# Kernel tuning notes

Measured on AMD Instinct MI355X. Metric: run time of the kernel, lower is better.

## Reference

```python
import jax, jax.numpy as jnp
import numpy as np
from jax.ops import segment_sum, segment_min, segment_max

N, E = 25000, 400000
NF, EF = 30, 10
H = 40          # n_hidden (multiple of towers)
T = 5           # towers
F = H           # F_in per tower (divide_input=False)
FO = H // T     # F_out per tower
L = 2           # gnn layers
NC = 2          # classes
EPS_BN = 1e-5


def setup_inputs() -> dict:
    key = jax.random.key(0)
    ks = jax.random.split(key, 24)
    r = lambda k, s, sc=0.1: jax.random.normal(k, s, jnp.float32) * sc
    return {
        "x": jax.random.normal(ks[0], (N, NF), jnp.float32),
        "edge_attr": jax.random.normal(ks[1], (E, EF), jnp.float32),
        "edge_index": jax.random.randint(ks[2], (2, E), 0, N, jnp.int32),
        "node_w": r(ks[3], (NF, H)), "node_b": r(ks[4], (H,)),
        "edge_w": r(ks[5], (EF, H)), "edge_b": r(ks[6], (H,)),
        "enc_w": r(ks[7], (L, H, F)), "enc_b": r(ks[8], (L, F)),
        "pre_w": r(ks[9], (L, T, 3 * F, F)), "pre_b": r(ks[10], (L, T, F)),
        "post_w": r(ks[11], (L, T, 13 * F, FO)), "post_b": r(ks[12], (L, T, FO)),
        "lin_w": r(ks[13], (L, H, H)), "lin_b": r(ks[14], (L, H)),
        "bn_g": jnp.ones((L, H), jnp.float32), "bn_b": jnp.zeros((L, H), jnp.float32),
        "mlp1_w": r(ks[15], (3 * H, 50)), "mlp1_b": r(ks[16], (50,)),
        "mlp2_w": r(ks[17], (50, 25)), "mlp2_b": r(ks[18], (25,)),
        "mlp3_w": r(ks[19], (25, NC)), "mlp3_b": r(ks[20], (NC,)),
    }


def _pna_conv(x, src, dst, e_emb, enc_w, enc_b, pre_w, pre_b, post_w, post_b,
              lin_w, lin_b, cnt, cnt1, amp, att):
    # message: per-tower pre-MLP on cat(x_i=dst, x_j=src, enc(edge_attr))
    e = e_emb @ enc_w + enc_b                                    # [E, F]
    h = jnp.concatenate([x[dst], x[src], e], axis=-1)            # [E, 3F]
    hs = jnp.einsum('ef,tfo->eto', h, pre_w) + pre_b             # [E, T, F]
    # multi-aggregation over incoming edges (index = dst)
    c = cnt1[:, None, None]
    mean = segment_sum(hs, dst, num_segments=N) / c
    msq = segment_sum(hs * hs, dst, num_segments=N) / c
    std = jnp.sqrt(jax.nn.relu(msq - mean * mean) + 1e-5)
    has = (cnt > 0)[:, None, None]
    mn = jnp.where(has, segment_min(hs, dst, num_segments=N), 0.0)
    mx = jnp.where(has, segment_max(hs, dst, num_segments=N), 0.0)
    agg = jnp.concatenate([mean, mn, mx, std], axis=-1)          # [N, T, 4F]
    agg = jnp.concatenate([agg, agg * amp, agg * att], axis=-1)  # [N, T, 12F]
    out = jnp.concatenate(
        [jnp.broadcast_to(x[:, None, :], (N, T, F)), agg], axis=-1)  # [N, T, 13F]
    out = jnp.einsum('ntf,tfo->nto', out, post_w) + post_b       # [N, T, FO]
    return out.reshape(N, T * FO) @ lin_w + lin_b                # [N, H]


def reference(x, edge_attr, node_w, node_b, edge_w, edge_b, enc_w, enc_b,
              pre_w, pre_b, post_w, post_b, lin_w, lin_b, bn_g, bn_b,
              mlp1_w, mlp1_b, mlp2_w, mlp2_b, mlp3_w, mlp3_b, edge_index):
    src, dst = edge_index[0], edge_index[1]
    cnt = segment_sum(jnp.ones((E,), jnp.float32), dst, num_segments=N)  # in-degree
    cnt1 = jnp.maximum(cnt, 1.0)                                 # deg.clamp_(1)
    log_deg = jnp.log(cnt1 + 1.0)
    avg_log = jnp.mean(jnp.log(cnt + 1.0))                       # PNA avg_deg['log']
    amp = (log_deg / avg_log)[:, None, None]
    att = (avg_log / log_deg)[:, None, None]
    h = x @ node_w + node_b                                      # node embedding
    e_emb = edge_attr @ edge_w + edge_b                          # edge embedding
    for i in range(L):
        c = _pna_conv(h, src, dst, e_emb, enc_w[i], enc_b[i], pre_w[i], pre_b[i],
                      post_w[i], post_b[i], lin_w[i], lin_b[i], cnt, cnt1, amp, att)
        mu = jnp.mean(c, axis=0)
        var = jnp.mean((c - mu) ** 2, axis=0)                    # BatchNorm (batch stats)
        cbn = (c - mu) / jnp.sqrt(var + EPS_BN) * bn_g[i] + bn_b[i]
        h = (h + jax.nn.relu(cbn)) / 2.0
    z = jax.nn.relu(jnp.concatenate([h[src], h[dst]], axis=-1))  # [E, 2H]
    z = jnp.concatenate([z, e_emb], axis=-1)                     # [E, 3H]
    z = jax.nn.relu(z @ mlp1_w + mlp1_b)
    z = jax.nn.relu(z @ mlp2_w + mlp2_b)
    return z @ mlp3_w + mlp3_b                                   # [E, NC]
```

## Files before the change

### kernel.cpp

```cpp
#include <hip/hip_runtime.h>
#include <hip/hip_bf16.h>
#include <cstdint>
#include <cstddef>

#define NN 25000
#define NE 400000
#define NFD 30
#define EFD 10
#define H 40
#define T 5
#define FO 8
#define LAYERS 2
#define TF 200
#define PSTR 52
#define REC 12
#define WCN 416
#define WCK 64
#define SHP 72
#define EPSV 1e-5f

typedef __attribute__((ext_vector_type(8))) short bf16x8;
typedef __attribute__((ext_vector_type(4))) float f32x4;

__device__ inline short bfbits(float v) {
    __hip_bfloat16 b = __float2bfloat16(v);
    return *(short*)&b;
}

__global__ __launch_bounds__(256) void k_deg(const int* __restrict__ dst, int* __restrict__ cnt) {
    int e = blockIdx.x * 256 + threadIdx.x;
    if (e < NE) atomicAdd(&cnt[dst[e]], 1);
}

__global__ __launch_bounds__(256) void k_avglog(const int* __restrict__ cnt, float* __restrict__ slot) {
    __shared__ float red[256];
    float s = 0.0f;
    for (int i = blockIdx.x * 256 + threadIdx.x; i < NN; i += gridDim.x * 256)
        s += logf((float)cnt[i] + 1.0f);
    red[threadIdx.x] = s; __syncthreads();
    for (int o = 128; o > 0; o >>= 1) {
        if (threadIdx.x < o) red[threadIdx.x] += red[threadIdx.x + o];
        __syncthreads();
    }
    if (threadIdx.x == 0) atomicAdd(slot, red[0]);
}

__global__ __launch_bounds__(256) void k_node(const float* __restrict__ x, const float* __restrict__ w,
                                              const float* __restrict__ b, float* __restrict__ h,
                                              const int* __restrict__ cnt, const float* __restrict__ slot,
                                              float* __restrict__ amp, float* __restrict__ att) {
    int id = blockIdx.x * 256 + threadIdx.x;
    if (id < NN) {
        float avg = slot[0] / (float)NN;
        float c1 = fmaxf((float)cnt[id], 1.0f);
        float lg = logf(c1 + 1.0f);
        amp[id] = lg / avg;
        att[id] = avg / lg;
    }
    if (id >= NN * H) return;
    int n = id / H, j = id - n * H;
    const float* xr = x + (size_t)n * NFD;
    float acc = b[j];
    #pragma unroll
    for (int m = 0; m < NFD; m++) acc += xr[m] * w[m * H + j];
    h[id] = acc;
}

__global__ __launch_bounds__(1024) void k_scan(const int* __restrict__ cnt, int* __restrict__ offs) {
    __shared__ int wsum[16];
    int tid = threadIdx.x;
    int lane = tid & 63, wv = tid >> 6;
    int runbase = 0;
    for (int base = 0; base < NN; base += 4096) {
        int i0 = base + tid * 4;
        int4 v = make_int4(0, 0, 0, 0);
        if (i0 < NN) v = *(const int4*)(cnt + i0);
        int tsum = v.x + v.y + v.z + v.w;
        int x = tsum;
        #pragma unroll
        for (int o = 1; o < 64; o <<= 1) {
            int y = __shfl_up(x, o);
            if (lane >= o) x += y;
        }
        if (lane == 63) wsum[wv] = x;
        __syncthreads();
        if (wv == 0 && lane < 16) {
            int wsv = wsum[lane];
            #pragma unroll
            for (int o = 1; o < 16; o <<= 1) {
                int y = __shfl_up(wsv, o);
                if (lane >= o) wsv += y;
            }
            wsum[lane] = wsv;
        }
        __syncthreads();
        int wpref = (wv > 0) ? wsum[wv - 1] : 0;
        int excl = runbase + wpref + x - tsum;
        if (i0 < NN) {
            offs[i0]     = excl;
            offs[i0 + 1] = excl + v.x;
            offs[i0 + 2] = excl + v.x + v.y;
            offs[i0 + 3] = excl + v.x + v.y + v.z;
        }
        runbase += wsum[15];
        __syncthreads();
    }
    if (tid == 0) offs[NN] = runbase;
}

__global__ __launch_bounds__(256) void k_scatter(const int* __restrict__ src, const int* __restrict__ dst,
                                                 const float* __restrict__ edge_attr,
                                                 const int* __restrict__ offs, int* __restrict__ fill,
                                                 float* __restrict__ ea_csr, int* __restrict__ pdst) {
    int e = blockIdx.x * 256 + threadIdx.x;
    if (e >= NE) return;
    int d = dst[e];
    int p = offs[d] + atomicAdd(&fill[d], 1);
    const float2* ear = (const float2*)(edge_attr + (size_t)e * EFD);
    float2 v0 = ear[0], v1 = ear[1], v2 = ear[2], v3 = ear[3], v4 = ear[4];
    float4* o = (float4*)(ea_csr + (size_t)p * REC);
    o[0] = make_float4(v0.x, v0.y, v1.x, v1.y);
    o[1] = make_float4(v2.x, v2.y, v3.x, v3.y);
    o[2] = make_float4(v4.x, v4.y, __int_as_float(src[e]), __int_as_float(e));
    pdst[p] = d;
}

__global__ __launch_bounds__(256) void k_prep1(const float* __restrict__ enc_w, const float* __restrict__ enc_b,
                                               const float* __restrict__ edge_w, const float* __restrict__ edge_b,
                                               const float* __restrict__ pre_w, const float* __restrict__ pre_b,
                                               const float* __restrict__ post_w,
                                               const float* __restrict__ w1, const float* __restrict__ b1,
                                               float* __restrict__ W3e, float* __restrict__ dvecF,
                                               __hip_bfloat16* __restrict__ Wcat,
                                               float* __restrict__ Wp4, float* __restrict__ Wxd,
                                               float* __restrict__ W1e, float* __restrict__ b1e, int layer) {
    int id = blockIdx.x * 256 + threadIdx.x;
    const int B0 = EFD * TF;
    const int B1 = B0 + WCN * WCK;
    const int B2 = B1 + EFD * 50;
    const int B3 = B2 + 40 * 512;
    const int B4 = B3 + H * H;
    if (id < B0) {
        int m = id / TF, j = id - m * TF;
        int t = j / H, f = j - t * H;
        const float* ew = enc_w + (size_t)layer * H * H;
        const float* pw = pre_w + (size_t)(layer * T + t) * 120 * H;
        float acc = 0.0f;
        for (int k = 0; k < H; k++) {
            float wk = edge_w[m * H + k];
            float g = 0.0f;
            #pragma unroll
            for (int o = 0; o < H; o++) g += ew[k * H + o] * pw[(80 + o) * H + f];
            acc += wk * g;
        }
        W3e[m * TF + j] = acc;
        if (m == 0) {
            const float* eb = enc_b + (size_t)layer * H;
            float dacc = pre_b[(size_t)(layer * T + t) * H + f];
            for (int o = 0; o < H; o++) {
                float ebe = eb[o];
                #pragma unroll
                for (int k = 0; k < H; k++) ebe += edge_b[k] * ew[k * H + o];
                dacc += ebe * pw[(80 + o) * H + f];
            }
            dvecF[j] = dacc;
        }
    } else if (id < B1) {
        int id2 = id - B0;
        int j = id2 / WCK, k = id2 - j * WCK;
        float val = 0.0f;
        if (k < H) {
            if (j < TF) {
                int t = j / H, f = j - t * H;
                val = pre_w[((size_t)(layer * T + t) * 120 + k) * H + f];
            } else if (j >= 208 && j < 208 + TF) {
                int j2 = j - 208;
                int t = j2 / H, f = j2 - t * H;
                val = pre_w[((size_t)(layer * T + t) * 120 + H + k) * H + f];
            }
        }
        Wcat[id2] = __float2bfloat16(val);
    } else if (id < B2) {
        if (layer == 0) {
            int id2 = id - B1;
            int m = id2 / 50, o = id2 - m * 50;
            float acc = 0.0f;
            #pragma unroll
            for (int k = 0; k < H; k++) acc += edge_w[m * H + k] * w1[(80 + k) * 50 + o];
            W1e[m * 50 + o] = acc;
            if (m == 0) {
                float bacc = b1[o];
                #pragma unroll
                for (int k = 0; k < H; k++) bacc += edge_b[k] * w1[(80 + k) * 50 + o];
                b1e[o] = bacc;
            }
        }
    } else if (id < B3) {
        int i2 = id - B2;
        int fs4 = i2 >> 9;
        int rem = i2 & 511;
        int col = rem >> 2, c = rem & 3;
        int fs = fs4 * 4 + c;
        float v = 0.0f;
        if (col < 120) {
            int t = col / 24, r2 = col - t * 24;
            int grp = r2 >> 3, o = r2 & 7;
            v = post_w[((size_t)(layer * T + t) * 520 + 40 + grp * 160 + fs) * FO + o];
        }
        Wp4[i2] = v;
    } else if (id < B4) {
        int i2 = id - B3;
        int j = i2 / H, f = i2 - j * H;
        int t = j >> 3, o = j & 7;
        Wxd[i2] = post_w[((size_t)(layer * T + t) * 520 + f) * FO + o];
    }
}

__global__ __launch_bounds__(256) void k_abm(float* h, const float* __restrict__ cbuf,
                                             const float* __restrict__ bnsum, const float* __restrict__ bnsq,
                                             const float* __restrict__ bng, const float* __restrict__ bnb,
                                             int doBN,
                                             const __hip_bfloat16* __restrict__ Wcat,
                                             float* __restrict__ A, __hip_bfloat16* __restrict__ Bbf) {
    __shared__ short sh[64 * SHP];
    int tid = threadIdx.x;
    int n0 = blockIdx.x * 64;
    int nodes = NN - n0; if (nodes > 64) nodes = 64;
    for (int i = tid; i < 64 * SHP; i += 256) sh[i] = 0;
    __syncthreads();
    float invN = 1.0f / (float)NN;
    for (int i = tid; i < nodes * H; i += 256) {
        int f = i % H;
        float hv = h[(size_t)n0 * H + i];
        float hn;
        if (doBN) {
            float mu = bnsum[f] * invN;
            float var = bnsq[f] * invN - mu * mu;
            float c = (cbuf[(size_t)n0 * H + i] - mu) * rsqrtf(var + EPSV) * bng[f] + bnb[f];
            hn = (hv + fmaxf(c, 0.0f)) * 0.5f;
            h[(size_t)n0 * H + i] = hn;
        } else {
            hn = hv;
        }
        sh[(i / H) * SHP + f] = bfbits(hn);
    }
    __syncthreads();

    int wv = tid >> 6, lane = tid & 63;
    int q = lane >> 4, c16 = lane & 15;
    const short* arow = sh + (wv * 16 + c16) * SHP + q * 8;
    bf16x8 a0 = *(const bf16x8*)(arow);
    bf16x8 a1 = *(const bf16x8*)(arow + 32);
    int gm = n0 + wv * 16 + q * 4;

    for (int jt = 0; jt < 26; jt++) {
        int col = jt * 16 + c16;
        const short* wrow = (const short*)Wcat + (size_t)col * WCK + q * 8;
        bf16x8 b0 = *(const bf16x8*)(wrow);
        bf16x8 b1 = *(const bf16x8*)(wrow + 32);
        f32x4 acc = {0.0f, 0.0f, 0.0f, 0.0f};
        acc = __builtin_amdgcn_mfma_f32_16x16x32_bf16(a0, b0, acc, 0, 0, 0);
        acc = __builtin_amdgcn_mfma_f32_16x16x32_bf16(a1, b1, acc, 0, 0, 0);
        if (col < TF) {
            #pragma unroll
            for (int r = 0; r < 4; r++) {
                int row = gm + r;
                if (row < NN) A[(size_t)row * TF + col] = acc[r];
            }
        } else if (col >= 208) {
            int c2 = col - 208;
            if (c2 < TF) {
                #pragma unroll
                for (int r = 0; r < 4; r++) {
                    int row = gm + r;
                    if (row < NN) Bbf[(size_t)row * TF + c2] = __float2bfloat16(acc[r]);
                }
            }
        }
    }
}

__global__ __launch_bounds__(256) void k_agg(const float* __restrict__ ea_csr,
                                             const __hip_bfloat16* __restrict__ Bbf,
                                             const float* __restrict__ A, const float* __restrict__ w3e,
                                             const float* __restrict__ dvecF, const int* __restrict__ cnt,
                                             const int* __restrict__ offs,
                                             const float* __restrict__ h,
                                             const float* __restrict__ Wp4, const float* __restrict__ Wxd,
                                             const float* __restrict__ pbL,
                                             const float* __restrict__ amp, const float* __restrict__ att,
                                             float* __restrict__ cpre) {
    __shared__ float sst[4 * 800];
    __shared__ float spart[4 * 120];
    __shared__ float shh[4 * H];
    int tid = threadIdx.x;
    int lane = tid & 63;
    int wv = tid >> 6;
    int n0 = blockIdx.x * 4;
    int n = __builtin_amdgcn_readfirstlane(n0 + wv);
    if (tid < 4 * H) shh[tid] = h[(size_t)n0 * H + tid];
    int deg = cnt[n];
    int start = offs[n];
    bool comp = lane < TF / 4;
    float4 w3q[EFD];
    float4 dj4 = make_float4(0, 0, 0, 0), a4 = make_float4(0, 0, 0, 0);
    if (comp) {
        #pragma unroll
        for (int m = 0; m < EFD; m++) w3q[m] = *(const float4*)(w3e + m * TF + 4 * lane);
        dj4 = *(const float4*)(dvecF + 4 * lane);
        a4  = *(const float4*)(A + (size_t)n * TF + 4 * lane);
    }
    float sx = 0, sy = 0, sz = 0, sw_ = 0;
    float qx = 0, qy = 0, qz = 0, qw = 0;
    float mnx = 3.4e38f, mny = 3.4e38f, mnz = 3.4e38f, mnw = 3.4e38f;
    float mxx = -3.4e38f, mxy = -3.4e38f, mxz = -3.4e38f, mxw = -3.4e38f;
    const float4* recb = (const float4*)ea_csr + (size_t)start * 3;
    const uint16_t* Bu = (const uint16_t*)Bbf;

    auto edge = [&](float4 qa, float4 qb, float4 qc, uint2 bv) {
        float b0 = __uint_as_float(bv.x << 16);
        float b1 = __uint_as_float(bv.x & 0xffff0000u);
        float b2 = __uint_as_float(bv.y << 16);
        float b3 = __uint_as_float(bv.y & 0xffff0000u);
        float eav[EFD] = {qa.x, qa.y, qa.z, qa.w, qb.x, qb.y, qb.z, qb.w, qc.x, qc.y};
        float cx = dj4.x, cy = dj4.y, cz = dj4.z, cw = dj4.w;
        #pragma unroll
        for (int m = 0; m < EFD; m++) {
            cx = fmaf(eav[m], w3q[m].x, cx);
            cy = fmaf(eav[m], w3q[m].y, cy);
            cz = fmaf(eav[m], w3q[m].z, cz);
            cw = fmaf(eav[m], w3q[m].w, cw);
        }
        float ux = b0 + cx, uy = b1 + cy, uz = b2 + cz, uw = b3 + cw;
        sx += ux; qx = fmaf(ux, ux, qx); mnx = fminf(mnx, ux); mxx = fmaxf(mxx, ux);
        sy += uy; qy = fmaf(uy, uy, qy); mny = fminf(mny, uy); mxy = fmaxf(mxy, uy);
        sz += uz; qz = fmaf(uz, uz, qz); mnz = fminf(mnz, uz); mxz = fmaxf(mxz, uz);
        sw_ += uw; qw = fmaf(uw, uw, qw); mnw = fminf(mnw, uw); mxw = fmaxf(mxw, uw);
    };

    int r = 0;
    for (; r + 4 <= deg; r += 4) {
        float4 qa0 = recb[(r + 0) * 3], qb0 = recb[(r + 0) * 3 + 1], qc0 = recb[(r + 0) * 3 + 2];
        float4 qa1 = recb[(r + 1) * 3], qb1 = recb[(r + 1) * 3 + 1], qc1 = recb[(r + 1) * 3 + 2];
        float4 qa2 = recb[(r + 2) * 3], qb2 = recb[(r + 2) * 3 + 1], qc2 = recb[(r + 2) * 3 + 2];
        float4 qa3 = recb[(r + 3) * 3], qb3 = recb[(r + 3) * 3 + 1], qc3 = recb[(r + 3) * 3 + 2];
        int s0 = __float_as_int(qc0.z), s1 = __float_as_int(qc1.z);
        int s2 = __float_as_int(qc2.z), s3 = __float_as_int(qc3.z);
        if (comp) {
            uint2 v0 = *(const uint2*)(Bu + (size_t)s0 * TF + 4 * lane);
            uint2 v1 = *(const uint2*)(Bu + (size_t)s1 * TF + 4 * lane);
            uint2 v2 = *(const uint2*)(Bu + (size_t)s2 * TF + 4 * lane);
            uint2 v3 = *(const uint2*)(Bu + (size_t)s3 * TF + 4 * lane);
            edge(qa0, qb0, qc0, v0);
            edge(qa1, qb1, qc1, v1);
            edge(qa2, qb2, qc2, v2);
            edge(qa3, qb3, qc3, v3);
        }
    }
    for (; r < deg; r++) {
        float4 qa = recb[r * 3], qb = recb[r * 3 + 1], qc = recb[r * 3 + 2];
        int sn = __float_as_int(qc.z);
        if (comp) {
            uint2 bv = *(const uint2*)(Bu + (size_t)sn * TF + 4 * lane);
            edge(qa, qb, qc, bv);
        }
    }
    if (comp) {
        float d = (float)deg, c1 = fmaxf(d, 1.0f);
        float inv = 1.0f / c1;
        float mex = (d * a4.x + sx) * inv, mey = (d * a4.y + sy) * inv;
        float mez = (d * a4.z + sz) * inv, mew = (d * a4.w + sw_) * inv;
        float msx = (d * a4.x * a4.x + 2.0f * a4.x * sx + qx) * inv;
        float msy = (d * a4.y * a4.y + 2.0f * a4.y * sy + qy) * inv;
        float msz = (d * a4.z * a4.z + 2.0f * a4.z * sz + qz) * inv;
        float msw = (d * a4.w * a4.w + 2.0f * a4.w * sw_ + qw) * inv;
        float4 mean4 = make_float4(mex, mey, mez, mew);
        float4 sd4 = make_float4(sqrtf(fmaxf(msx - mex * mex, 0.0f) + EPSV),
                                 sqrtf(fmaxf(msy - mey * mey, 0.0f) + EPSV),
                                 sqrtf(fmaxf(msz - mez * mez, 0.0f) + EPSV),
                                 sqrtf(fmaxf(msw - mew * mew, 0.0f) + EPSV));
        bool has = deg > 0;
        float4 mnv4 = has ? make_float4(a4.x + mnx, a4.y + mny, a4.z + mnz, a4.w + mnw)
                          : make_float4(0, 0, 0, 0);
        float4 mxv4 = has ? make_float4(a4.x + mxx, a4.y + mxy, a4.z + mxz, a4.w + mxw)
                          : make_float4(0, 0, 0, 0);
        int j0 = 4 * lane;
        int t = j0 / H, f = j0 - t * H;
        float* sb = sst + wv * 800 + t * 160 + f;
        *(float4*)(sb)       = mean4;
        *(float4*)(sb + 40)  = mnv4;
        *(float4*)(sb + 80)  = mxv4;
        *(float4*)(sb + 120) = sd4;
    }
    __syncthreads();

    {
        int op = tid & 127, g = tid >> 7;
        int tt = op / 24; if (tt > 4) tt = 4;
        const float* sa = sst + (g * 2) * 800 + tt * 160;
        const float* sb = sa + 800;
        float pa = 0.0f, pb = 0.0f;
        #pragma unroll 4
        for (int fs4 = 0; fs4 < 40; fs4++) {
            float4 w  = *(const float4*)(Wp4 + fs4 * 512 + op * 4);
            float4 va = *(const float4*)(sa + fs4 * 4);
            float4 vb = *(const float4*)(sb + fs4 * 4);
            pa += va.x * w.x + va.y * w.y + va.z * w.z + va.w * w.w;
            pb += vb.x * w.x + vb.y * w.y + vb.z * w.z + vb.w * w.w;
        }
        if (op < 120) {
            spart[(g * 2) * 120 + op]     = pa;
            spart[(g * 2 + 1) * 120 + op] = pb;
        }
    }
    __syncthreads();

    if (tid < 160) {
        int nd = tid / H, j = tid - nd * H;
        int t = j >> 3, o = j & 7;
        int ng = n0 + nd;
        float am = amp[ng], at = att[ng];
        const float* yr = spart + nd * 120 + t * 24 + o;
        float acc = pbL[j] + yr[0] + am * yr[8] + at * yr[16];
        const float* hr = shh + nd * H;
        const float* wx = Wxd + (size_t)j * H;
        #pragma unroll
        for (int fq = 0; fq < 10; fq++) {
            float4 hv = *(const float4*)(hr + fq * 4);
            float4 wv = *(const float4*)(wx + fq * 4);
            acc += hv.x * wv.x + hv.y * wv.y + hv.z * wv.z + hv.w * wv.w;
        }
        cpre[(size_t)ng * H + j] = acc;
    }
}

__global__ __launch_bounds__(256) void k_linbn(const float* __restrict__ cpre, const float* __restrict__ lin_w,
                                               const float* __restrict__ lin_b, float* __restrict__ cbuf,
                                               float* __restrict__ bnsum, float* __restrict__ bnsq, int layer) {
    __shared__ float scp[240];
    __shared__ float red[80];
    int tid = threadIdx.x;
    int j = tid % H, nl = tid / H;
    const float* lw = lin_w + (size_t)layer * H * H;
    float wcol[H];
    #pragma unroll
    for (int k = 0; k < H; k++) wcol[k] = lw[k * H + j];
    float lb = lin_b[(size_t)layer * H + j];
    float lsum = 0.0f, lsq = 0.0f;
    for (int n0 = blockIdx.x * 6; n0 < NN; n0 += gridDim.x * 6) {
        int nn = NN - n0; if (nn > 6) nn = 6;
        if (tid < nn * H) scp[tid] = cpre[(size_t)n0 * H + tid];
        __syncthreads();
        if (nl < nn) {
            float acc = lb;
            #pragma unroll
            for (int k = 0; k < H; k++) acc += scp[nl * H + k] * wcol[k];
            cbuf[(size_t)(n0 + nl) * H + j] = acc;
            lsum += acc; lsq += acc * acc;
        }
        __syncthreads();
    }
    if (tid < 80) red[tid] = 0.0f;
    __syncthreads();
    if (nl < 6) { atomicAdd(&red[j], lsum); atomicAdd(&red[40 + j], lsq); }
    __syncthreads();
    if (tid < 40) atomicAdd(&bnsum[tid], red[tid]);
    else if (tid < 80) atomicAdd(&bnsq[tid - 40], red[tid]);
}

__global__ __launch_bounds__(256) void k_prep2(const float* __restrict__ h, const float* __restrict__ cbuf,
                                               const float* __restrict__ bnsum, const float* __restrict__ bnsq,
                                               const float* __restrict__ bng, const float* __restrict__ bnb,
                                               const float* __restrict__ w1,
                                               float* __restrict__ P1, float* __restrict__ P2) {
    __shared__ float sh[5 * H];
    int tid = threadIdx.x;
    int n0 = blockIdx.x * 5;
    if (tid < 5 * H) {
        int j = tid % H;
        float invN = 1.0f / (float)NN;
        float mu = bnsum[j] * invN;
        float var = bnsq[j] * invN - mu * mu;
        float inv = rsqrtf(var + EPSV);
        float cv = (cbuf[(size_t)n0 * H + tid] - mu) * inv * bng[j] + bnb[j];
        sh[tid] = (h[(size_t)n0 * H + tid] + fmaxf(cv, 0.0f)) * 0.5f;
    }
    __syncthreads();
    if (tid >= 250) return;
    int nl = tid / 50, o = tid - nl * 50;
    const float* hr = sh + nl * H;
    float a1 = 0.0f, a2 = 0.0f;
    #pragma unroll
    for (int f = 0; f < H; f++) {
        float v = fmaxf(hr[f], 0.0f);
        a1 += v * w1[f * 50 + o];
        a2 += v * w1[(H + f) * 50 + o];
    }
    P1[(size_t)(n0 + nl) * PSTR + o] = a1;
    P2[(size_t)(n0 + nl) * PSTR + o] = a2;
}

__global__ __launch_bounds__(256) void k_mlp(const float* __restrict__ ea_csr, const int* __restrict__ pdst,
                                             const float* __restrict__ P1, const float* __restrict__ P2,
                                             const float* __restrict__ W1e, const float* __restrict__ b1e,
                                             const float* __restrict__ w2, const float* __restrict__ b2,
                                             const float* __restrict__ w3, const float* __restrict__ b3,
                                             float* __restrict__ out) {
    int p = blockIdx.x * 256 + threadIdx.x;
    if (p >= NE) return;
    const float4* rec = (const float4*)ea_csr + (size_t)p * 3;
    float4 r0 = rec[0], r1 = rec[1], r2 = rec[2];
    int s = __float_as_int(r2.z), eid = __float_as_int(r2.w);
    int d = pdst[p];
    float ea[EFD] = {r0.x, r0.y, r0.z, r0.w, r1.x, r1.y, r1.z, r1.w, r2.x, r2.y};

    float z1[52];
    const float4* p1r = (const float4*)(P1 + (size_t)s * PSTR);
    const float4* p2r = (const float4*)(P2 + (size_t)d * PSTR);
    #pragma unroll
    for (int i = 0; i < 13; i++) {
        float4 a = p1r[i], b = p2r[i];
        z1[4 * i]     = a.x + b.x;
        z1[4 * i + 1] = a.y + b.y;
        z1[4 * i + 2] = a.z + b.z;
        z1[4 * i + 3] = a.w + b.w;
    }
    #pragma unroll
    for (int k = 0; k < 50; k++) z1[k] += b1e[k];
    #pragma unroll
    for (int m = 0; m < EFD; m++) {
        float v = ea[m];
        #pragma unroll
        for (int k = 0; k < 50; k++) z1[k] = fmaf(v, W1e[m * 50 + k], z1[k]);
    }
    float z2[25];
    #pragma unroll
    for (int o = 0; o < 25; o++) z2[o] = b2[o];
    #pragma unroll
    for (int k = 0; k < 50; k++) {
        float v = fmaxf(z1[k], 0.0f);
        #pragma unroll
        for (int o = 0; o < 25; o++) z2[o] = fmaf(v, w2[k * 25 + o], z2[o]);
    }
    float o0 = b3[0], o1 = b3[1];
    #pragma unroll
    for (int k = 0; k < 25; k++) {
        float v = fmaxf(z2[k], 0.0f);
        o0 = fmaf(v, w3[k * 2], o0);
        o1 = fmaf(v, w3[k * 2 + 1], o1);
    }
    *(float2*)(out + (size_t)eid * 2) = make_float2(o0, o1);
}

extern "C" void kernel_launch(void* const* d_in, const int* in_sizes, int n_in,
                              void* d_out, int out_size, void* d_ws, size_t ws_size,
                              hipStream_t stream) {
    const float* x         = (const float*)d_in[0];
    const float* edge_attr = (const float*)d_in[1];
    const int*   eidx      = (const int*)  d_in[2];
    const float* node_w    = (const float*)d_in[3];
    const float* node_b    = (const float*)d_in[4];
    const float* edge_w    = (const float*)d_in[5];
    const float* edge_b    = (const float*)d_in[6];
    const float* enc_w     = (const float*)d_in[7];
    const float* enc_b     = (const float*)d_in[8];
    const float* pre_w     = (const float*)d_in[9];
    const float* pre_b     = (const float*)d_in[10];
    const float* post_w    = (const float*)d_in[11];
    const float* post_b    = (const float*)d_in[12];
    const float* lin_w     = (const float*)d_in[13];
    const float* lin_b     = (const float*)d_in[14];
    const float* bn_g      = (const float*)d_in[15];
    const float* bn_b      = (const float*)d_in[16];
    const float* w1 = (const float*)d_in[17];
    const float* b1 = (const float*)d_in[18];
    const float* w2 = (const float*)d_in[19];
    const float* b2 = (const float*)d_in[20];
    const float* w3 = (const float*)d_in[21];
    const float* b3 = (const float*)d_in[22];
    const int* srcp = eidx;
    const int* dstp = eidx + NE;
    float* out = (float*)d_out;

    char* ws = (char*)d_ws;
    size_t off = 0;
    auto alloc = [&](size_t bytes) -> char* {
        char* p = ws + off;
        off += (bytes + 255) & ~(size_t)255;
        return p;
    };
    float* h      = (float*)alloc((size_t)NN * H * 4);
    float* Abuf   = (float*)alloc((size_t)NN * TF * 4);
    float* cbuf   = (float*)alloc((size_t)NN * H * 4);
    __hip_bfloat16* Bbf = (__hip_bfloat16*)alloc((size_t)NN * TF * 2 + 256);
    float* cpre   = (float*)alloc((size_t)NN * H * 4);
    float* ea_csr = (float*)alloc((size_t)NE * REC * 4);
    int* pdst     = (int*)alloc((size_t)NE * 4);
    float* W3e    = (float*)alloc((size_t)EFD * TF * 4);
    float* dvecF  = (float*)alloc((size_t)TF * 4);
    __hip_bfloat16* Wcat = (__hip_bfloat16*)alloc((size_t)WCN * WCK * 2);
    float* Wp4    = (float*)alloc((size_t)40 * 512 * 4);
    float* Wxd    = (float*)alloc((size_t)H * H * 4);
    float* P1     = (float*)alloc((size_t)NN * PSTR * 4);
    float* P2     = (float*)alloc((size_t)NN * PSTR * 4);
    float* W1e    = (float*)alloc((size_t)EFD * 50 * 4);
    float* b1e    = (float*)alloc((size_t)64 * 4);
    float* amp    = (float*)alloc((size_t)NN * 4);
    float* att    = (float*)alloc((size_t)NN * 4);
    int* offs     = (int*)alloc((size_t)(NN + 1) * 4);
    size_t zoff = off;
    int* cnt_i    = (int*)alloc((size_t)NN * 4);
    int* fill     = (int*)alloc((size_t)NN * 4);
    float* avgs   = (float*)alloc(256);
    float* bnz    = (float*)alloc(1024);
    size_t zsize = off - zoff;
    if (off > ws_size) return;

    hipMemsetAsync(cnt_i, 0, zsize, stream);

    k_deg<<<(NE + 255) / 256, 256, 0, stream>>>(dstp, cnt_i);
    k_avglog<<<64, 256, 0, stream>>>(cnt_i, avgs);
    k_node<<<(NN * H + 255) / 256, 256, 0, stream>>>(x, node_w, node_b, h, cnt_i, avgs, amp, att);
    k_scan<<<1, 1024, 0, stream>>>(cnt_i, offs);
    k_scatter<<<(NE + 255) / 256, 256, 0, stream>>>(srcp, dstp, edge_attr, offs, fill, ea_csr, pdst);

    int prep1_tot = EFD * TF + WCN * WCK + EFD * 50 + 40 * 512 + H * H;
    int prep1_grid = (prep1_tot + 255) / 256;
    for (int layer = 0; layer < LAYERS; layer++) {
        float* bnzL = bnz + layer * 128;
        k_prep1<<<prep1_grid, 256, 0, stream>>>(
            enc_w, enc_b, edge_w, edge_b, pre_w, pre_b, post_w, w1, b1,
            W3e, dvecF, Wcat, Wp4, Wxd, W1e, b1e, layer);
        float* bnzP = bnz + (layer - 1) * 128;
        k_abm<<<(NN + 63) / 64, 256, 0, stream>>>(
            h, cbuf, (layer > 0) ? bnzP : bnz, (layer > 0) ? bnzP + 40 : bnz,
            bn_g + (size_t)(layer > 0 ? layer - 1 : 0) * H,
            bn_b + (size_t)(layer > 0 ? layer - 1 : 0) * H,
            (layer > 0) ? 1 : 0, Wcat, Abuf, Bbf);
        k_agg<<<NN / 4, 256, 0, stream>>>(ea_csr, Bbf, Abuf, W3e, dvecF, cnt_i, offs,
                                          h, Wp4, Wxd, post_b + (size_t)layer * T * FO,
                                          amp, att, cpre);
        k_linbn<<<1024, 256, 0, stream>>>(cpre, lin_w, lin_b, cbuf, bnzL, bnzL + 40, layer);
    }
    k_prep2<<<NN / 5, 256, 0, stream>>>(h, cbuf, bnz + 128, bnz + 168,
                                        bn_g + H, bn_b + H, w1, P1, P2);
    k_mlp<<<(NE + 255) / 256, 256, 0, stream>>>(ea_csr, pdst, P1, P2, W1e, b1e, w2, b2, w3, b3, out);
}
```

Baseline: 583.8 us.

## Process eight nodes per aggregation block to amortize post-MLP weight loads

The aggregation kernel now has each wavefront handle two destination nodes in sequence, so a block covers eight nodes instead of four. The post-tower weight matrix Wp4 is then read once per eight nodes, with the K dimension split across two thread halves and partial sums reduced through shared memory reused from the stats buffer. The cost is serialized per-wave edge loops, which means less latency hiding from parallel nodes. Shared memory also grows, and fewer blocks are launched, which could lower occupancy.

Result: no change. 586.1 us (+0.4%).

```diff
diff --git a/kernel.cpp b/kernel.cpp
--- a/kernel.cpp
+++ b/kernel.cpp
@@ -17,6 +17,7 @@
 #define WCN 416
 #define WCK 64
 #define SHP 72
+#define NPB 8
 #define EPSV 1e-5f
 
 typedef __attribute__((ext_vector_type(8))) short bf16x8;
@@ -290,138 +291,165 @@
                                              const float* __restrict__ pbL,
                                              const float* __restrict__ amp, const float* __restrict__ att,
                                              float* __restrict__ cpre) {
-    __shared__ float sst[4 * 800];
-    __shared__ float spart[4 * 120];
-    __shared__ float shh[4 * H];
+    __shared__ float sst[NPB * 800];
+    __shared__ float shh[NPB * H];
+    float* spart = sst;
     int tid = threadIdx.x;
     int lane = tid & 63;
     int wv = tid >> 6;
-    int n0 = blockIdx.x * 4;
-    int n = __builtin_amdgcn_readfirstlane(n0 + wv);
-    if (tid < 4 * H) shh[tid] = h[(size_t)n0 * H + tid];
-    int deg = cnt[n];
-    int start = offs[n];
+    int n0 = blockIdx.x * NPB;
+    for (int idx = tid; idx < NPB * H; idx += 256) shh[idx] = h[(size_t)n0 * H + idx];
     bool comp = lane < TF / 4;
     float4 w3q[EFD];
-    float4 dj4 = make_float4(0, 0, 0, 0), a4 = make_float4(0, 0, 0, 0);
+    float4 dj4 = make_float4(0, 0, 0, 0);
     if (comp) {
         #pragma unroll
         for (int m = 0; m < EFD; m++) w3q[m] = *(const float4*)(w3e + m * TF + 4 * lane);
         dj4 = *(const float4*)(dvecF + 4 * lane);
-        a4  = *(const float4*)(A + (size_t)n * TF + 4 * lane);
-    }
-    float sx = 0, sy = 0, sz = 0, sw_ = 0;
-    float qx = 0, qy = 0, qz = 0, qw = 0;
-    float mnx = 3.4e38f, mny = 3.4e38f, mnz = 3.4e38f, mnw = 3.4e38f;
-    float mxx = -3.4e38f, mxy = -3.4e38f, mxz = -3.4e38f, mxw = -3.4e38f;
-    const float4* recb = (const float4*)ea_csr + (size_t)start * 3;
+    }
     const uint16_t* Bu = (const uint16_t*)Bbf;
 
-    auto edge = [&](float4 qa, float4 qb, float4 qc, uint2 bv) {
-        float b0 = __uint_as_float(bv.x << 16);
-        float b1 = __uint_as_float(bv.x & 0xffff0000u);
-        float b2 = __uint_as_float(bv.y << 16);
-        float b3 = __uint_as_float(bv.y & 0xffff0000u);
-        float eav[EFD] = {qa.x, qa.y, qa.z, qa.w, qb.x, qb.y, qb.z, qb.w, qc.x, qc.y};
-        float cx = dj4.x, cy = dj4.y, cz = dj4.z, cw = dj4.w;
-        #pragma unroll
-        for (int m = 0; m < EFD; m++) {
-            cx = fmaf(eav[m], w3q[m].x, cx);
-            cy = fmaf(eav[m], w3q[m].y, cy);
-            cz = fmaf(eav[m], w3q[m].z, cz);
-            cw = fmaf(eav[m], w3q[m].w, cw);
-        }
-        float ux = b0 + cx, uy = b1 + cy, uz = b2 + cz, uw = b3 + cw;
-        sx += ux; qx = fmaf(ux, ux, qx); mnx = fminf(mnx, ux); mxx = fmaxf(mxx, ux);
-        sy += uy; qy = fmaf(uy, uy, qy); mny = fminf(mny, uy); mxy = fmaxf(mxy, uy);
-        sz += uz; qz = fmaf(uz, uz, qz); mnz = fminf(mnz, uz); mxz = fmaxf(mxz, uz);
-        sw_ += uw; qw = fmaf(uw, uw, qw); mnw = fminf(mnw, uw); mxw = fmaxf(mxw, uw);
-    };
-
-    int r = 0;
-    for (; r + 4 <= deg; r += 4) {
-        float4 qa0 = recb[(r + 0) * 3], qb0 = recb[(r + 0) * 3 + 1], qc0 = recb[(r + 0) * 3 + 2];
-        float4 qa1 = recb[(r + 1) * 3], qb1 = recb[(r + 1) * 3 + 1], qc1 = recb[(r + 1) * 3 + 2];
-        float4 qa2 = recb[(r + 2) * 3], qb2 = recb[(r + 2) * 3 + 1], qc2 = recb[(r + 2) * 3 + 2];
-        float4 qa3 = recb[(r + 3) * 3], qb3 = recb[(r + 3) * 3 + 1], qc3 = recb[(r + 3) * 3 + 2];
-        int s0 = __float_as_int(qc0.z), s1 = __float_as_int(qc1.z);
-        int s2 = __float_as_int(qc2.z), s3 = __float_as_int(qc3.z);
+    for (int i = 0; i < 2; i++) {
+        int n = __builtin_amdgcn_readfirstlane(n0 + wv * 2 + i);
+        int deg = cnt[n];
+        int start = offs[n];
+        float4 a4 = make_float4(0, 0, 0, 0);
+        if (comp) a4 = *(const float4*)(A + (size_t)n * TF + 4 * lane);
+        float sx = 0, sy = 0, sz = 0, sw_ = 0;
+        float qx = 0, qy = 0, qz = 0, qw = 0;
+        float mnx = 3.4e38f, mny = 3.4e38f, mnz = 3.4e38f, mnw = 3.4e38f;
+        float mxx = -3.4e38f, mxy = -3.4e38f, mxz = -3.4e38f, mxw = -3.4e38f;
+        const float4* recb = (const float4*)ea_csr + (size_t)start * 3;
+
+        auto edge = [&](float4 qa, float4 qb, float4 qc, uint2 bv) {
+            float b0 = __uint_as_float(bv.x << 16);
+            float b1 = __uint_as_float(bv.x & 0xffff0000u);
+            float b2 = __uint_as_float(bv.y << 16);
+            float b3 = __uint_as_float(bv.y & 0xffff0000u);
+            float eav[EFD] = {qa.x, qa.y, qa.z, qa.w, qb.x, qb.y, qb.z, qb.w, qc.x, qc.y};
+            float cx = dj4.x, cy = dj4.y, cz = dj4.z, cw = dj4.w;
+            #pragma unroll
+            for (int m = 0; m < EFD; m++) {
+                cx = fmaf(eav[m], w3q[m].x, cx);
+                cy = fmaf(eav[m], w3q[m].y, cy);
+                cz = fmaf(eav[m], w3q[m].z, cz);
+                cw = fmaf(eav[m], w3q[m].w, cw);
+            }
+            float ux = b0 + cx, uy = b1 + cy, uz = b2 + cz, uw = b3 + cw;
+            sx += ux; qx = fmaf(ux, ux, qx); mnx = fminf(mnx, ux); mxx = fmaxf(mxx, ux);
+            sy += uy; qy = fmaf(uy, uy, qy); mny = fminf(mny, uy); mxy = fmaxf(mxy, uy);
+            sz += uz; qz = fmaf(uz, uz, qz); mnz = fminf(mnz, uz); mxz = fmaxf(mxz, uz);
+            sw_ += uw; qw = fmaf(uw, uw, qw); mnw = fminf(mnw, uw); mxw = fmaxf(mxw, uw);
+        };
+
+        int r = 0;
+        for (; r + 4 <= deg; r += 4) {
+            float4 qa0 = recb[(r + 0) * 3], qb0 = recb[(r + 0) * 3 + 1], qc0 = recb[(r + 0) * 3 + 2];
+            float4 qa1 = recb[(r + 1) * 3], qb1 = recb[(r + 1) * 3 + 1], qc1 = recb[(r + 1) * 3 + 2];
+            float4 qa2 = recb[(r + 2) * 3], qb2 = recb[(r + 2) * 3 + 1], qc2 = recb[(r + 2) * 3 + 2];
+            float4 qa3 = recb[(r + 3) * 3], qb3 = recb[(r + 3) * 3 + 1], qc3 = recb[(r + 3) * 3 + 2];
+            int s0 = __float_as_int(qc0.z), s1 = __float_as_int(qc1.z);
+            int s2 = __float_as_int(qc2.z), s3 = __float_as_int(qc3.z);
+            if (comp) {
+                uint2 v0 = *(const uint2*)(Bu + (size_t)s0 * TF + 4 * lane);
+                uint2 v1 = *(const uint2*)(Bu + (size_t)s1 * TF + 4 * lane);
+                uint2 v2 = *(const uint2*)(Bu + (size_t)s2 * TF + 4 * lane);
+                uint2 v3 = *(const uint2*)(Bu + (size_t)s3 * TF + 4 * lane);
+                edge(qa0, qb0, qc0, v0);
+                edge(qa1, qb1, qc1, v1);
+                edge(qa2, qb2, qc2, v2);
+                edge(qa3, qb3, qc3, v3);
+            }
+        }
+        for (; r < deg; r++) {
+            float4 qa = recb[r * 3], qb = recb[r * 3 + 1], qc = recb[r * 3 + 2];
+            int sn = __float_as_int(qc.z);
+            if (comp) {
+                uint2 bv = *(const uint2*)(Bu + (size_t)sn * TF + 4 * lane);
+                edge(qa, qb, qc, bv);
+            }
+        }
         if (comp) {
-            uint2 v0 = *(const uint2*)(Bu + (size_t)s0 * TF + 4 * lane);
-            uint2 v1 = *(const uint2*)(Bu + (size_t)s1 * TF + 4 * lane);
-            uint2 v2 = *(const uint2*)(Bu + (size_t)s2 * TF + 4 * lane);
-            uint2 v3 = *(const uint2*)(Bu + (size_t)s3 * TF + 4 * lane);
-            edge(qa0, qb0, qc0, v0);
-            edge(qa1, qb1, qc1, v1);
-            edge(qa2, qb2, qc2, v2);
-            edge(qa3, qb3, qc3, v3);
-        }
-    }
-    for (; r < deg; r++) {
-        float4 qa = recb[r * 3], qb = recb[r * 3 + 1], qc = recb[r * 3 + 2];
-        int sn = __float_as_int(qc.z);
-        if (comp) {
-            uint2 bv = *(const uint2*)(Bu + (size_t)sn * TF + 4 * lane);
-            edge(qa, qb, qc, bv);
-        }
-    }
-    if (comp) {
-        float d = (float)deg, c1 = fmaxf(d, 1.0f);
-        float inv = 1.0f / c1;
-        float mex = (d * a4.x + sx) * inv, mey = (d * a4.y + sy) * inv;
-        float mez = (d * a4.z + sz) * inv, mew = (d * a4.w + sw_) * inv;
-        float msx = (d * a4.x * a4.x + 2.0f * a4.x * sx + qx) * inv;
-        float msy = (d * a4.y * a4.y + 2.0f * a4.y * sy + qy) * inv;
-        float msz = (d * a4.z * a4.z + 2.0f * a4.z * sz + qz) * inv;
-        float msw = (d * a4.w * a4.w + 2.0f * a4.w * sw_ + qw) * inv;
-        float4 mean4 = make_float4(mex, mey, mez, mew);
-        float4 sd4 = make_float4(sqrtf(fmaxf(msx - mex * mex, 0.0f) + EPSV),
-                                 sqrtf(fmaxf(msy - mey * mey, 0.0f) + EPSV),
-                                 sqrtf(fmaxf(msz - mez * mez, 0.0f) + EPSV),
-                                 sqrtf(fmaxf(msw - mew * mew, 0.0f) + EPSV));
-        bool has = deg > 0;
-        float4 mnv4 = has ? make_float4(a4.x + mnx, a4.y + mny, a4.z + mnz, a4.w + mnw)
-                          : make_float4(0, 0, 0, 0);
-        float4 mxv4 = has ? make_float4(a4.x + mxx, a4.y + mxy, a4.z + mxz, a4.w + mxw)
-                          : make_float4(0, 0, 0, 0);
-        int j0 = 4 * lane;
-        int t = j0 / H, f = j0 - t * H;
-        float* sb = sst + wv * 800 + t * 160 + f;
-        *(float4*)(sb)       = mean4;
-        *(float4*)(sb + 40)  = mnv4;
-        *(float4*)(sb + 80)  = mxv4;
-        *(float4*)(sb + 120) = sd4;
+            float d = (float)deg, c1 = fmaxf(d, 1.0f);
+            float inv = 1.0f / c1;
+            float mex = (d * a4.x + sx) * inv, mey = (d * a4.y + sy) * inv;
+            float mez = (d * a4.z + sz) * inv, mew = (d * a4.w + sw_) * inv;
+            float msx = (d * a4.x * a4.x + 2.0f * a4.x * sx + qx) * inv;
+            float msy = (d * a4.y * a4.y + 2.0f * a4.y * sy + qy) * inv;
+            float msz = (d * a4.z * a4.z + 2.0f * a4.z * sz + qz) * inv;
+            float msw = (d * a4.w * a4.w + 2.0f * a4.w * sw_ + qw) * inv;
+            float4 mean4 = make_float4(mex, mey, mez, mew);
+            float4 sd4 = make_float4(sqrtf(fmaxf(msx - mex * mex, 0.0f) + EPSV),
+                                     sqrtf(fmaxf(msy - mey * mey, 0.0f) + EPSV),
+                                     sqrtf(fmaxf(msz - mez * mez, 0.0f) + EPSV),
+                                     sqrtf(fmaxf(msw - mew * mew, 0.0f) + EPSV));
+            bool has = deg > 0;
+            float4 mnv4 = has ? make_float4(a4.x + mnx, a4.y + mny, a4.z + mnz, a4.w + mnw)
+                              : make_float4(0, 0, 0, 0);
+            float4 mxv4 = has ? make_float4(a4.x + mxx, a4.y + mxy, a4.z + mxz, a4.w + mxw)
+                              : make_float4(0, 0, 0, 0);
+            int j0 = 4 * lane;
+            int t = j0 / H, f = j0 - t * H;
+            float* sb = sst + (wv * 2 + i) * 800 + t * 160 + f;
+            *(float4*)(sb)       = mean4;
+            *(float4*)(sb + 40)  = mnv4;
+            *(float4*)(sb + 80)  = mxv4;
+            *(float4*)(sb + 120) = sd4;
+        }
     }
     __syncthreads();
 
     {
-        int op = tid & 127, g = tid >> 7;
+        int op = tid & 127, half = tid >> 7;
         int tt = op / 24; if (tt > 4) tt = 4;
-        const float* sa = sst + (g * 2) * 800 + tt * 160;
-        const float* sb = sa + 800;
-        float pa = 0.0f, pb = 0.0f;
+        const float* wtp = Wp4 + (size_t)(half * 20) * 512 + op * 4;
+        const float* sb0 = sst + tt * 160 + half * 80;
+        float p0 = 0, p1 = 0, p2 = 0, p3 = 0, p4 = 0, p5 = 0, p6 = 0, p7 = 0;
         #pragma unroll 4
-        for (int fs4 = 0; fs4 < 40; fs4++) {
-            float4 w  = *(const float4*)(Wp4 + fs4 * 512 + op * 4);
-            float4 va = *(const float4*)(sa + fs4 * 4);
-            float4 vb = *(const float4*)(sb + fs4 * 4);
-            pa += va.x * w.x + va.y * w.y + va.z * w.z + va.w * w.w;
-            pb += vb.x * w.x + vb.y * w.y + vb.z * w.z + vb.w * w.w;
-        }
+        for (int k = 0; k < 20; k++) {
+            float4 w = *(const float4*)(wtp + k * 512);
+            const float* sp = sb0 + k * 4;
+            float4 v0 = *(const float4*)(sp);
+            float4 v1 = *(const float4*)(sp + 800);
+            float4 v2 = *(const float4*)(sp + 1600);
+            float4 v3 = *(const float4*)(sp + 2400);
+            float4 v4 = *(const float4*)(sp + 3200);
+            float4 v5 = *(const float4*)(sp + 4000);
+            float4 v6 = *(const float4*)(sp + 4800);
+            float4 v7 = *(const float4*)(sp + 5600);
+            p0 += v0.x * w.x + v0.y * w.y + v0.z * w.z + v0.w * w.w;
+            p1 += v1.x * w.x + v1.y * w.y + v1.z * w.z + v1.w * w.w;
+            p2 += v2.x * w.x + v2.y * w.y + v2.z * w.z + v2.w * w.w;
+            p3 += v3.x * w.x + v3.y * w.y + v3.z * w.z + v3.w * w.w;
+            p4 += v4.x * w.x + v4.y * w.y + v4.z * w.z + v4.w * w.w;
+            p5 += v5.x * w.x + v5.y * w.y + v5.z * w.z + v5.w * w.w;
+            p6 += v6.x * w.x + v6.y * w.y + v6.z * w.z + v6.w * w.w;
+            p7 += v7.x * w.x + v7.y * w.y + v7.z * w.z + v7.w * w.w;
+        }
+        __syncthreads();
         if (op < 120) {
-            spart[(g * 2) * 120 + op]     = pa;
-            spart[(g * 2 + 1) * 120 + op] = pb;
+            spart[(0 * 120 + op) * 2 + half] = p0;
+            spart[(1 * 120 + op) * 2 + half] = p1;
+            spart[(2 * 120 + op) * 2 + half] = p2;
+            spart[(3 * 120 + op) * 2 + half] = p3;
+            spart[(4 * 120 + op) * 2 + half] = p4;
+            spart[(5 * 120 + op) * 2 + half] = p5;
+            spart[(6 * 120 + op) * 2 + half] = p6;
+            spart[(7 * 120 + op) * 2 + half] = p7;
         }
     }
     __syncthreads();
 
-    if (tid < 160) {
-        int nd = tid / H, j = tid - nd * H;
+    for (int idx = tid; idx < NPB * H; idx += 256) {
+        int nd = idx / H, j = idx - nd * H;
         int t = j >> 3, o = j & 7;
         int ng = n0 + nd;
         float am = amp[ng], at = att[ng];
-        const float* yr = spart + nd * 120 + t * 24 + o;
-        float acc = pbL[j] + yr[0] + am * yr[8] + at * yr[16];
+        const float* yr = spart + (nd * 120 + t * 24) * 2;
+        float pa = yr[o * 2]        + yr[o * 2 + 1];
+        float pb = yr[(8 + o) * 2]  + yr[(8 + o) * 2 + 1];
+        float pc = yr[(16 + o) * 2] + yr[(16 + o) * 2 + 1];
+        float acc = pbL[j] + pa + am * pb + at * pc;
         const float* hr = shh + nd * H;
         const float* wx = Wxd + (size_t)j * H;
         #pragma unroll
@@ -637,9 +665,9 @@
             bn_g + (size_t)(layer > 0 ? layer - 1 : 0) * H,
             bn_b + (size_t)(layer > 0 ? layer - 1 : 0) * H,
             (layer > 0) ? 1 : 0, Wcat, Abuf, Bbf);
-        k_agg<<<NN / 4, 256, 0, stream>>>(ea_csr, Bbf, Abuf, W3e, dvecF, cnt_i, offs,
-                                          h, Wp4, Wxd, post_b + (size_t)layer * T * FO,
-                                          amp, att, cpre);
+        k_agg<<<NN / NPB, 256, 0, stream>>>(ea_csr, Bbf, Abuf, W3e, dvecF, cnt_i, offs,
+                                            h, Wp4, Wxd, post_b + (size_t)layer * T * FO,
+                                            amp, att, cpre);
         k_linbn<<<1024, 256, 0, stream>>>(cpre, lin_w, lin_b, cbuf, bnzL, bnzL + 40, layer);
     }
     k_prep2<<<NN / 5, 256, 0, stream>>>(h, cbuf, bnz + 128, bnz + 168,
```
